# Kernel tuning notes

Measured on AMD Instinct MI355X. Metric: run time of the kernel, lower is better.

Reference implementation:

```python
import jax, jax.numpy as jnp
import numpy as np

N_NODES = 50000
N_EDGES = 800000
D = 128
N_LAYERS = 4


def _sage_conv(x, edge_index, Wl, bl, Wr):
    # PyG SAGEConv (mean aggr): out = lin_l(mean_{j in N(i)} x_j) + lin_r(x_i)
    src, dst = edge_index[0], edge_index[1]
    msgs = x[src]                                            # [E, D] gather
    summed = jax.ops.segment_sum(msgs, dst, num_segments=N_NODES)   # [N, D]
    cnt = jax.ops.segment_sum(jnp.ones((msgs.shape[0],), x.dtype), dst,
                              num_segments=N_NODES)
    mean = summed / jnp.maximum(cnt, 1.0)[:, None]           # [N, D]
    return mean @ Wl.T + bl + x @ Wr.T


def setup_inputs() -> dict:
    key = jax.random.key(0)
    ks = jax.random.split(key, 2 + 3 * N_LAYERS)
    x = jax.random.normal(ks[0], (N_NODES, D), dtype=jnp.float32)
    edge_index = jax.random.randint(ks[1], (2, N_EDGES), 0, N_NODES, dtype=jnp.int64)
    inp = {"x": x, "edge_index": edge_index}
    s = 1.0 / np.sqrt(D)
    for i in range(N_LAYERS):
        inp[f"Wl{i}"] = jax.random.uniform(ks[2 + 3 * i], (D, D), jnp.float32, -s, s)
        inp[f"bl{i}"] = jax.random.uniform(ks[3 + 3 * i], (D,), jnp.float32, -s, s)
        inp[f"Wr{i}"] = jax.random.uniform(ks[4 + 3 * i], (D, D), jnp.float32, -s, s)
    return inp


def reference(x, edge_index, Wl0, bl0, Wr0, Wl1, bl1, Wr1, Wl2, bl2, Wr2, Wl3, bl3, Wr3):
    # ReLU only after the first conv, per the original forward.
    h = jax.nn.relu(_sage_conv(x, edge_index, Wl0, bl0, Wr0))
    h = _sage_conv(h, edge_index, Wl1, bl1, Wr1)
    h = _sage_conv(h, edge_index, Wl2, bl2, Wr2)
    h = _sage_conv(h, edge_index, Wl3, bl3, Wr3)
    return h
```

## Files before the change

kernel.cpp:

```cpp
#include <hip/hip_runtime.h>
#include <stdint.h>

#define NN 50000
#define NE 800000
#define CAST_B 6250
#define CVTW_B 512
#define EPB 8192
#define HIST_B 98
#define NBK 196

typedef short short8 __attribute__((ext_vector_type(8)));
typedef float f32x4 __attribute__((ext_vector_type(4)));
typedef unsigned int uint;
typedef unsigned short ushort;

__device__ __forceinline__ uint rne_bf16(float f) {
    uint x = __float_as_uint(f);
    return (x + 0x7FFFu + ((x >> 16) & 1u)) >> 16;
}
__device__ __forceinline__ float bf_lo(uint d) { return __uint_as_float(d << 16); }
__device__ __forceinline__ float bf_hi(uint d) { return __uint_as_float(d & 0xFFFF0000u); }

__device__ __forceinline__ int ei_is64(const int* __restrict__ ei) {
    return (ei[1] | ei[3] | ei[5] | ei[7]) == 0;
}

struct Ptrs8 { const float* p[8]; };

__global__ __launch_bounds__(256) void k_prep(
    const float* __restrict__ x, ushort* __restrict__ xbf, Ptrs8 ps,
    ushort* __restrict__ wbf, const int* __restrict__ ei,
    uint* __restrict__ ebuf, int* __restrict__ hcnt) {
    __shared__ int hs[NBK];
    int b = blockIdx.x;
    if (b < CAST_B) {
        int i = b * 256 + threadIdx.x;
        float4 v = ((const float4*)x)[i];
        uint2 o;
        o.x = rne_bf16(v.x) | (rne_bf16(v.y) << 16);
        o.y = rne_bf16(v.z) | (rne_bf16(v.w) << 16);
        ((uint2*)xbf)[i] = o;
    } else if (b < CAST_B + CVTW_B) {
        int idx = (b - CAST_B) * 256 + threadIdx.x;
        int m = idx >> 14;
        int off = idx & 16383;
        wbf[idx] = (ushort)rne_bf16(ps.p[m][off]);
    } else {
        int hb = b - CAST_B - CVTW_B;
        int t = threadIdx.x;
        for (int i = t; i < NBK; i += 256) hs[i] = 0;
        __syncthreads();
        int base = hb * EPB;
        int is64 = ei_is64(ei);
        for (int i = 0; i < EPB; i += 256) {
            int e = base + i + t;
            if (e < NE) {
                int sv = is64 ? ei[2 * e] : ei[e];
                int dv = is64 ? ei[2 * NE + 2 * e] : ei[NE + e];
                ebuf[e] = ((uint)dv << 16) | (uint)sv;
                atomicAdd(&hs[dv >> 8], 1);
            }
        }
        __syncthreads();
        for (int i = t; i < NBK; i += 256) hcnt[hb * NBK + i] = hs[i];
    }
}

__global__ __launch_bounds__(256) void k_scan1(const int* __restrict__ hcnt,
                                               int* __restrict__ hoff,
                                               int* __restrict__ bb,
                                               int* __restrict__ row_ptr) {
    __shared__ int s[256];
    int t = threadIdx.x;
    int tot = 0;
    if (t < NBK)
        for (int b = 0; b < HIST_B; b++) tot += hcnt[b * NBK + t];
    s[t] = tot;
    __syncthreads();
    for (int off = 1; off < 256; off <<= 1) {
        int v = s[t];
        int a = (t >= off) ? s[t - off] : 0;
        __syncthreads();
        s[t] = v + a;
        __syncthreads();
    }
    if (t < NBK) {
        int base = (t == 0) ? 0 : s[t - 1];
        bb[t] = base;
        int run = base;
        for (int b = 0; b < HIST_B; b++) {
            hoff[b * NBK + t] = run;
            run += hcnt[b * NBK + t];
        }
    }
    if (t == 0) { bb[NBK] = NE; row_ptr[NN] = NE; }
}

__global__ __launch_bounds__(256) void k_scatter1(const uint* __restrict__ ebuf,
                                                  const int* __restrict__ hoff,
                                                  uint* __restrict__ ebuf2) {
    __shared__ int pos[NBK];
    int hb = blockIdx.x, t = threadIdx.x;
    for (int i = t; i < NBK; i += 256) pos[i] = hoff[hb * NBK + i];
    __syncthreads();
    int base = hb * EPB;
    for (int i = 0; i < EPB; i += 256) {
        int e = base + i + t;
        if (e < NE) {
            uint pk = ebuf[e];
            int idx = atomicAdd(&pos[pk >> 24], 1);
            ebuf2[idx] = pk;
        }
    }
}

__global__ __launch_bounds__(1024) void k_sort2(const uint* __restrict__ ebuf2,
                                                const int* __restrict__ bb,
                                                int* __restrict__ row_ptr,
                                                ushort* __restrict__ col) {
    __shared__ int hist[256];
    __shared__ int pos[256];
    int k = blockIdx.x, t = threadIdx.x;
    int beg = bb[k], end = bb[k + 1];
    if (t < 256) hist[t] = 0;
    __syncthreads();
    for (int j = beg + t; j < end; j += 1024)
        atomicAdd(&hist[(ebuf2[j] >> 16) & 255], 1);
    __syncthreads();
    for (int off = 1; off < 256; off <<= 1) {
        int v = 0;
        if (t < 256) { v = hist[t]; if (t >= off) v += hist[t - off]; }
        __syncthreads();
        if (t < 256) hist[t] = v;
        __syncthreads();
    }
    if (t < 256) {
        int ex = (t == 0) ? 0 : hist[t - 1];
        pos[t] = beg + ex;
        int node = k * 256 + t;
        if (node < NN) row_ptr[node] = beg + ex;
    }
    __syncthreads();
    for (int j = beg + t; j < end; j += 1024) {
        uint pk = ebuf2[j];
        int idx = atomicAdd(&pos[(pk >> 16) & 255], 1);
        col[idx] = (ushort)(pk & 0xFFFFu);
    }
}

__global__ __launch_bounds__(256) void k_agg3(const ushort* __restrict__ h,
                                              const int* __restrict__ row_ptr,
                                              const ushort* __restrict__ col,
                                              ushort* __restrict__ mean) {
    int node = blockIdx.x * 4 + (threadIdx.x >> 6);
    if (node >= NN) return;
    int lane = threadIdx.x & 63;
    int beg = row_ptr[node], end = row_ptr[node + 1];
    const uint* hp = (const uint*)h;
    float a0 = 0.f, a1 = 0.f;
    for (int b = beg; b < end; b += 64) {
        int n = min(64, end - b);
        int c = (int)col[b + min(lane, n - 1)];
        for (int j0 = 0; j0 < n; j0 += 8) {
#pragma unroll
            for (int j = 0; j < 8; j++) {
                int jj = j0 + j;
                int s = __shfl(c, min(jj, n - 1));
                uint v = hp[s * 64 + lane];
                float m = (jj < n) ? 1.f : 0.f;
                a0 = fmaf(m, bf_lo(v), a0);
                a1 = fmaf(m, bf_hi(v), a1);
            }
        }
    }
    float r = 1.0f / (float)max(end - beg, 1);
    ((uint*)mean)[node * 64 + lane] = rne_bf16(a0 * r) | (rne_bf16(a1 * r) << 16);
}

__global__ __launch_bounds__(256) void k_gemm_mfma(
    const ushort* __restrict__ Am, const ushort* __restrict__ Ah,
    const ushort* __restrict__ Wlb, const ushort* __restrict__ Wrb,
    const float* __restrict__ bias, float* __restrict__ outf,
    ushort* __restrict__ outb, int relu) {
    const int lane = threadIdx.x & 63;
    const int wave = threadIdx.x >> 6;
    const int l15 = lane & 15;
    const int quad = lane >> 4;
    const int m0 = blockIdx.x * 64 + wave * 16;

    f32x4 acc[8];
#pragma unroll
    for (int t = 0; t < 8; t++) acc[t] = (f32x4){0.f, 0.f, 0.f, 0.f};

    int arow = min(m0 + l15, NN - 1);
    const ushort* Arm = Am + (size_t)arow * 128 + quad * 8;
    const ushort* Arh = Ah + (size_t)arow * 128 + quad * 8;
    const int wro = quad * 8;

#pragma unroll
    for (int half = 0; half < 2; half++) {
        const ushort* Ar = half ? Arh : Arm;
        const ushort* W = half ? Wrb : Wlb;
#pragma unroll
        for (int k0 = 0; k0 < 128; k0 += 32) {
            short8 a = *(const short8*)(Ar + k0);
#pragma unroll
            for (int t = 0; t < 8; t++) {
                short8 b = *(const short8*)(W + (size_t)(t * 16 + l15) * 128 + k0 + wro);
                acc[t] = __builtin_amdgcn_mfma_f32_16x16x32_bf16(a, b, acc[t], 0, 0, 0);
            }
        }
    }

    float bb[8];
#pragma unroll
    for (int t = 0; t < 8; t++) bb[t] = bias[t * 16 + l15];

#pragma unroll
    for (int r = 0; r < 4; r++) {
        int row = m0 + quad * 4 + r;
        if (row < NN) {
#pragma unroll
            for (int t = 0; t < 8; t++) {
                float v = acc[t][r] + bb[t];
                if (relu) v = fmaxf(v, 0.f);
                if (outb) outb[(size_t)row * 128 + t * 16 + l15] = (ushort)rne_bf16(v);
                else outf[(size_t)row * 128 + t * 16 + l15] = v;
            }
        }
    }
}

extern "C" void kernel_launch(void* const* d_in, const int* in_sizes, int n_in,
                              void* d_out, int out_size, void* d_ws, size_t ws_size,
                              hipStream_t stream) {
    const float* x = (const float*)d_in[0];
    const int* ei = (const int*)d_in[1];
    const float* Wl[4] = {(const float*)d_in[2], (const float*)d_in[5],
                          (const float*)d_in[8], (const float*)d_in[11]};
    const float* bl[4] = {(const float*)d_in[3], (const float*)d_in[6],
                          (const float*)d_in[9], (const float*)d_in[12]};
    const float* Wr[4] = {(const float*)d_in[4], (const float*)d_in[7],
                          (const float*)d_in[10], (const float*)d_in[13]};
    float* out = (float*)d_out;

    char* p = (char*)d_ws;
    auto take = [&](size_t bytes) -> char* {
        char* r = p;
        p += (bytes + 255) & ~(size_t)255;
        return r;
    };
    uint* ebuf = (uint*)take((size_t)NE * 4);
    uint* ebuf2 = (uint*)take((size_t)NE * 4);
    int* hcnt = (int*)take((size_t)HIST_B * NBK * 4);
    int* hoff = (int*)take((size_t)HIST_B * NBK * 4);
    int* bb = (int*)take((NBK + 1) * 4);
    int* row_ptr = (int*)take((NN + 1) * 4);
    ushort* col = (ushort*)take((size_t)NE * 2 + 256);
    ushort* xbf = (ushort*)take((size_t)NN * 128 * 2);
    ushort* h1 = (ushort*)take((size_t)NN * 128 * 2);
    ushort* h2 = (ushort*)take((size_t)NN * 128 * 2);
    ushort* meanbf = (ushort*)take((size_t)NN * 128 * 2);
    ushort* wbf = (ushort*)take(8 * 16384 * 2);

    Ptrs8 ps;
    ps.p[0] = Wl[0]; ps.p[1] = Wr[0]; ps.p[2] = Wl[1]; ps.p[3] = Wr[1];
    ps.p[4] = Wl[2]; ps.p[5] = Wr[2]; ps.p[6] = Wl[3]; ps.p[7] = Wr[3];

    k_prep<<<CAST_B + CVTW_B + HIST_B, 256, 0, stream>>>(x, xbf, ps, wbf, ei,
                                                         ebuf, hcnt);
    k_scan1<<<1, 256, 0, stream>>>(hcnt, hoff, bb, row_ptr);
    k_scatter1<<<HIST_B, 256, 0, stream>>>(ebuf, hoff, ebuf2);
    k_sort2<<<NBK, 1024, 0, stream>>>(ebuf2, bb, row_ptr, col);

    const ushort* h = xbf;
    ushort* houts[4] = {h1, h2, h1, nullptr};
    for (int l = 0; l < 4; l++) {
        k_agg3<<<(NN + 3) / 4, 256, 0, stream>>>(h, row_ptr, col, meanbf);
        k_gemm_mfma<<<(NN + 63) / 64, 256, 0, stream>>>(
            meanbf, h, wbf + (size_t)(2 * l) * 16384,
            wbf + (size_t)(2 * l + 1) * 16384, bl[l], out, houts[l],
            l == 0 ? 1 : 0);
        h = houts[l];
    }
}
```

Before: 406.3 us.

## Pre-swizzle bf16 weights into MFMA fragment order and compute two row tiles per wave

The weight conversion now writes each bf16 weight matrix in the exact per-lane fragment order the 16x16x32 MFMA consumes, so each B load becomes one contiguous 16-byte read per lane instead of a strided row gather. Each wave now computes 32 output rows (two 16-row tiles) and reuses every loaded B fragment for both tiles, which halves weight traffic per output row and halves the GEMM grid. In exchange it doubles the accumulator registers per wave and launches fewer blocks, which may reduce occupancy and latency hiding on the GEMM kernel.

```diff
diff --git a/kernel.cpp b/kernel.cpp
--- a/kernel.cpp
+++ b/kernel.cpp
@@ -43,8 +43,14 @@
     } else if (b < CAST_B + CVTW_B) {
         int idx = (b - CAST_B) * 256 + threadIdx.x;
         int m = idx >> 14;
-        int off = idx & 16383;
-        wbf[idx] = (ushort)rne_bf16(ps.p[m][off]);
+        int o14 = idx & 16383;
+        int k0i = (o14 >> 12) & 3;
+        int t = (o14 >> 9) & 7;
+        int lane6 = (o14 >> 3) & 63;
+        int e = o14 & 7;
+        int r = t * 16 + (lane6 & 15);
+        int c = k0i * 32 + (lane6 >> 4) * 8 + e;
+        wbf[idx] = (ushort)rne_bf16(ps.p[m][r * 128 + c]);
     } else {
         int hb = b - CAST_B - CVTW_B;
         int t = threadIdx.x;
@@ -186,28 +192,36 @@
     const int wave = threadIdx.x >> 6;
     const int l15 = lane & 15;
     const int quad = lane >> 4;
-    const int m0 = blockIdx.x * 64 + wave * 16;
-
-    f32x4 acc[8];
-#pragma unroll
-    for (int t = 0; t < 8; t++) acc[t] = (f32x4){0.f, 0.f, 0.f, 0.f};
-
-    int arow = min(m0 + l15, NN - 1);
-    const ushort* Arm = Am + (size_t)arow * 128 + quad * 8;
-    const ushort* Arh = Ah + (size_t)arow * 128 + quad * 8;
-    const int wro = quad * 8;
+    const int m0 = blockIdx.x * 128 + wave * 32;
+
+    f32x4 acc[2][8];
+#pragma unroll
+    for (int s = 0; s < 2; s++)
+#pragma unroll
+        for (int t = 0; t < 8; t++) acc[s][t] = (f32x4){0.f, 0.f, 0.f, 0.f};
+
+    int ar0 = min(m0 + l15, NN - 1);
+    int ar1 = min(m0 + 16 + l15, NN - 1);
+    const ushort* A0m = Am + (size_t)ar0 * 128 + quad * 8;
+    const ushort* A1m = Am + (size_t)ar1 * 128 + quad * 8;
+    const ushort* A0h = Ah + (size_t)ar0 * 128 + quad * 8;
+    const ushort* A1h = Ah + (size_t)ar1 * 128 + quad * 8;
 
 #pragma unroll
     for (int half = 0; half < 2; half++) {
-        const ushort* Ar = half ? Arh : Arm;
         const ushort* W = half ? Wrb : Wlb;
+        const ushort* A0 = half ? A0h : A0m;
+        const ushort* A1 = half ? A1h : A1m;
 #pragma unroll
         for (int k0 = 0; k0 < 128; k0 += 32) {
-            short8 a = *(const short8*)(Ar + k0);
+            short8 a0 = *(const short8*)(A0 + k0);
+            short8 a1 = *(const short8*)(A1 + k0);
+            const ushort* Wk = W + ((k0 >> 5) * 8) * 512 + lane * 8;
 #pragma unroll
             for (int t = 0; t < 8; t++) {
-                short8 b = *(const short8*)(W + (size_t)(t * 16 + l15) * 128 + k0 + wro);
-                acc[t] = __builtin_amdgcn_mfma_f32_16x16x32_bf16(a, b, acc[t], 0, 0, 0);
+                short8 b = *(const short8*)(Wk + t * 512);
+                acc[0][t] = __builtin_amdgcn_mfma_f32_16x16x32_bf16(a0, b, acc[0][t], 0, 0, 0);
+                acc[1][t] = __builtin_amdgcn_mfma_f32_16x16x32_bf16(a1, b, acc[1][t], 0, 0, 0);
             }
         }
     }
@@ -217,15 +231,18 @@
     for (int t = 0; t < 8; t++) bb[t] = bias[t * 16 + l15];
 
 #pragma unroll
-    for (int r = 0; r < 4; r++) {
-        int row = m0 + quad * 4 + r;
-        if (row < NN) {
-#pragma unroll
-            for (int t = 0; t < 8; t++) {
-                float v = acc[t][r] + bb[t];
-                if (relu) v = fmaxf(v, 0.f);
-                if (outb) outb[(size_t)row * 128 + t * 16 + l15] = (ushort)rne_bf16(v);
-                else outf[(size_t)row * 128 + t * 16 + l15] = v;
+    for (int s = 0; s < 2; s++) {
+#pragma unroll
+        for (int r = 0; r < 4; r++) {
+            int row = m0 + s * 16 + quad * 4 + r;
+            if (row < NN) {
+#pragma unroll
+                for (int t = 0; t < 8; t++) {
+                    float v = acc[s][t][r] + bb[t];
+                    if (relu) v = fmaxf(v, 0.f);
+                    if (outb) outb[(size_t)row * 128 + t * 16 + l15] = (ushort)rne_bf16(v);
+                    else outf[(size_t)row * 128 + t * 16 + l15] = v;
+                }
             }
         }
     }
@@ -277,7 +294,7 @@
     ushort* houts[4] = {h1, h2, h1, nullptr};
     for (int l = 0; l < 4; l++) {
         k_agg3<<<(NN + 3) / 4, 256, 0, stream>>>(h, row_ptr, col, meanbf);
-        k_gemm_mfma<<<(NN + 63) / 64, 256, 0, stream>>>(
+        k_gemm_mfma<<<(NN + 127) / 128, 256, 0, stream>>>(
             meanbf, h, wbf + (size_t)(2 * l) * 16384,
             wbf + (size_t)(2 * l + 1) * 16384, bl[l], out, houts[l],
             l == 0 ? 1 : 0);
```

Measured after the change: 353.6 us. 1.15x faster.

## Fuse neighbor aggregation into MFMA GEMM via LDS and pre-swizzle weights

Applied to the files above, without the earlier changes.

Each block now aggregates the mean neighbor features for its 64 nodes directly into shared memory and then runs the bf16 MFMA GEMM from LDS. This removes the separate aggregation kernel, the global mean buffer write and read, and one launch per layer. The weight conversion also reorders the weights into the MFMA fragment layout so B loads are contiguous per lane. The cost is parallelism: the gather phase now uses 782 blocks of 4 waves, each wave handling 16 nodes serially, instead of one wave per node across 12500 blocks, which may reduce latency hiding in the memory-bound gather.

```diff
diff --git a/kernel.cpp b/kernel.cpp
--- a/kernel.cpp
+++ b/kernel.cpp
@@ -8,6 +8,7 @@
 #define EPB 8192
 #define HIST_B 98
 #define NBK 196
+#define FUSE_B 782
 
 typedef short short8 __attribute__((ext_vector_type(8)));
 typedef float f32x4 __attribute__((ext_vector_type(4)));
@@ -43,8 +44,14 @@
     } else if (b < CAST_B + CVTW_B) {
         int idx = (b - CAST_B) * 256 + threadIdx.x;
         int m = idx >> 14;
-        int off = idx & 16383;
-        wbf[idx] = (ushort)rne_bf16(ps.p[m][off]);
+        int o14 = idx & 16383;
+        int k0i = (o14 >> 12) & 3;
+        int t = (o14 >> 9) & 7;
+        int lane6 = (o14 >> 3) & 63;
+        int e = o14 & 7;
+        int r = t * 16 + (lane6 & 15);
+        int c = k0i * 32 + (lane6 >> 4) * 8 + e;
+        wbf[idx] = (ushort)rne_bf16(ps.p[m][r * 128 + c]);
     } else {
         int hb = b - CAST_B - CVTW_B;
         int t = threadIdx.x;
@@ -148,65 +155,67 @@
     }
 }
 
-__global__ __launch_bounds__(256) void k_agg3(const ushort* __restrict__ h,
-                                              const int* __restrict__ row_ptr,
-                                              const ushort* __restrict__ col,
-                                              ushort* __restrict__ mean) {
-    int node = blockIdx.x * 4 + (threadIdx.x >> 6);
-    if (node >= NN) return;
-    int lane = threadIdx.x & 63;
-    int beg = row_ptr[node], end = row_ptr[node + 1];
+__global__ __launch_bounds__(256) void k_fused(
+    const ushort* __restrict__ h, const int* __restrict__ row_ptr,
+    const ushort* __restrict__ col, const ushort* __restrict__ Wlb,
+    const ushort* __restrict__ Wrb, const float* __restrict__ bias,
+    float* __restrict__ outf, ushort* __restrict__ outb, int relu) {
+    __shared__ uint smean[64 * 68];
+    const int wid = threadIdx.x >> 6;
+    const int lane = threadIdx.x & 63;
+    const int m0 = blockIdx.x * 64;
     const uint* hp = (const uint*)h;
-    float a0 = 0.f, a1 = 0.f;
-    for (int b = beg; b < end; b += 64) {
-        int n = min(64, end - b);
-        int c = (int)col[b + min(lane, n - 1)];
-        for (int j0 = 0; j0 < n; j0 += 8) {
-#pragma unroll
-            for (int j = 0; j < 8; j++) {
-                int jj = j0 + j;
-                int s = __shfl(c, min(jj, n - 1));
-                uint v = hp[s * 64 + lane];
-                float m = (jj < n) ? 1.f : 0.f;
-                a0 = fmaf(m, bf_lo(v), a0);
-                a1 = fmaf(m, bf_hi(v), a1);
-            }
-        }
-    }
-    float r = 1.0f / (float)max(end - beg, 1);
-    ((uint*)mean)[node * 64 + lane] = rne_bf16(a0 * r) | (rne_bf16(a1 * r) << 16);
-}
-
-__global__ __launch_bounds__(256) void k_gemm_mfma(
-    const ushort* __restrict__ Am, const ushort* __restrict__ Ah,
-    const ushort* __restrict__ Wlb, const ushort* __restrict__ Wrb,
-    const float* __restrict__ bias, float* __restrict__ outf,
-    ushort* __restrict__ outb, int relu) {
-    const int lane = threadIdx.x & 63;
-    const int wave = threadIdx.x >> 6;
+
+    for (int ni = 0; ni < 16; ni++) {
+        int rl = wid * 16 + ni;
+        int node = m0 + rl;
+        if (node < NN) {
+            int beg = row_ptr[node], end = row_ptr[node + 1];
+            float a0 = 0.f, a1 = 0.f;
+            for (int b = beg; b < end; b += 64) {
+                int n = min(64, end - b);
+                int c = (int)col[b + min(lane, n - 1)];
+                for (int j0 = 0; j0 < n; j0 += 8) {
+#pragma unroll
+                    for (int j = 0; j < 8; j++) {
+                        int jj = j0 + j;
+                        int s = __shfl(c, min(jj, n - 1));
+                        uint v = hp[s * 64 + lane];
+                        float m = (jj < n) ? 1.f : 0.f;
+                        a0 = fmaf(m, bf_lo(v), a0);
+                        a1 = fmaf(m, bf_hi(v), a1);
+                    }
+                }
+            }
+            float r = 1.0f / (float)max(end - beg, 1);
+            smean[rl * 68 + lane] = rne_bf16(a0 * r) | (rne_bf16(a1 * r) << 16);
+        } else {
+            smean[rl * 68 + lane] = 0;
+        }
+    }
+    __syncthreads();
+
     const int l15 = lane & 15;
     const int quad = lane >> 4;
-    const int m0 = blockIdx.x * 64 + wave * 16;
-
     f32x4 acc[8];
 #pragma unroll
     for (int t = 0; t < 8; t++) acc[t] = (f32x4){0.f, 0.f, 0.f, 0.f};
 
-    int arow = min(m0 + l15, NN - 1);
-    const ushort* Arm = Am + (size_t)arow * 128 + quad * 8;
-    const ushort* Arh = Ah + (size_t)arow * 128 + quad * 8;
-    const int wro = quad * 8;
+    int arow = min(m0 + wid * 16 + l15, NN - 1);
+    const ushort* Arh = h + (size_t)arow * 128 + quad * 8;
+    const uint* Alds = &smean[(wid * 16 + l15) * 68 + quad * 4];
 
 #pragma unroll
     for (int half = 0; half < 2; half++) {
-        const ushort* Ar = half ? Arh : Arm;
         const ushort* W = half ? Wrb : Wlb;
 #pragma unroll
         for (int k0 = 0; k0 < 128; k0 += 32) {
-            short8 a = *(const short8*)(Ar + k0);
+            short8 a = half ? *(const short8*)(Arh + k0)
+                            : *(const short8*)(Alds + (k0 >> 1));
+            const ushort* Wk = W + ((k0 >> 5) * 8) * 512 + lane * 8;
 #pragma unroll
             for (int t = 0; t < 8; t++) {
-                short8 b = *(const short8*)(W + (size_t)(t * 16 + l15) * 128 + k0 + wro);
+                short8 b = *(const short8*)(Wk + t * 512);
                 acc[t] = __builtin_amdgcn_mfma_f32_16x16x32_bf16(a, b, acc[t], 0, 0, 0);
             }
         }
@@ -218,7 +227,7 @@
 
 #pragma unroll
     for (int r = 0; r < 4; r++) {
-        int row = m0 + quad * 4 + r;
+        int row = m0 + wid * 16 + quad * 4 + r;
         if (row < NN) {
 #pragma unroll
             for (int t = 0; t < 8; t++) {
@@ -260,7 +269,6 @@
     ushort* xbf = (ushort*)take((size_t)NN * 128 * 2);
     ushort* h1 = (ushort*)take((size_t)NN * 128 * 2);
     ushort* h2 = (ushort*)take((size_t)NN * 128 * 2);
-    ushort* meanbf = (ushort*)take((size_t)NN * 128 * 2);
     ushort* wbf = (ushort*)take(8 * 16384 * 2);
 
     Ptrs8 ps;
@@ -276,9 +284,8 @@
     const ushort* h = xbf;
     ushort* houts[4] = {h1, h2, h1, nullptr};
     for (int l = 0; l < 4; l++) {
-        k_agg3<<<(NN + 3) / 4, 256, 0, stream>>>(h, row_ptr, col, meanbf);
-        k_gemm_mfma<<<(NN + 63) / 64, 256, 0, stream>>>(
-            meanbf, h, wbf + (size_t)(2 * l) * 16384,
+        k_fused<<<FUSE_B, 256, 0, stream>>>(
+            h, row_ptr, col, wbf + (size_t)(2 * l) * 16384,
             wbf + (size_t)(2 * l + 1) * 16384, bl[l], out, houts[l],
             l == 0 ? 1 : 0);
         h = houts[l];
```

After: 361.7 us. -11.0%, faster.
